# Optimization experiments

Measured on AMD Instinct MI355X. Metric: run time of the kernel, lower is better.

## Reference

```python
import jax, jax.numpy as jnp
import numpy as np

B, L, C = 2, 8192, 1536
P, W, H, F = 512, 16, 32, 128
POS = 32  # pos_channels (even, half=16 <= P-1)
EPS = 1e-5


def central_mask_features(seq_len, feat):
    # static numpy construction (matches torch central_mask_features)
    half = feat // 2
    rel = np.arange(2 * seq_len - 1, dtype=np.float64) - (seq_len - 1)
    widths = np.arange(half, dtype=np.float64) + np.geomspace(1, seq_len - half + 1, half, endpoint=False)
    onehot = (widths[None, :] > np.abs(rel)[:, None]).astype(np.float32)
    sign = np.sign(rel)[:, None].astype(np.float32)
    return jnp.asarray(np.concatenate([onehot, onehot * sign], axis=-1))  # [2P-1, POS]


def relative_shift(x):
    # x: [B, H, S, 2S-1] -> [B, H, S, S]
    b, h, s, d = x.shape
    x = jnp.pad(x, ((0, 0), (0, 0), (0, 0), (1, 0)))
    x = x.reshape(b, h, d + 1, s)[:, :, 1:, :].reshape(b, h, s, d)
    return x[..., :s]


def setup_inputs() -> dict:
    key = jax.random.key(0)
    ks = jax.random.split(key, 12)
    s = 0.02
    return {
        "x": jax.random.normal(ks[0], (B, L, C), jnp.float32),
        "norm_scale": jnp.ones((C,), jnp.float32),
        "norm_ms": jnp.ones((C,), jnp.float32),
        "Wq": jax.random.normal(ks[1], (C, H * F), jnp.float32) * s,
        "Wk": jax.random.normal(ks[2], (C, H * F), jnp.float32) * s,
        "Wp": jax.random.normal(ks[3], (POS, H * F), jnp.float32) * s,
        "bp": jax.random.normal(ks[4], (H * F,), jnp.float32) * s,
        "q_r_bias": jnp.zeros((1, 1, H, F), jnp.float32),
        "k_r_bias": jnp.zeros((1, 1, H, F), jnp.float32),
        "Wyq": jax.random.normal(ks[5], (C, F), jnp.float32) * s,
        "Wyk": jax.random.normal(ks[6], (C, F), jnp.float32) * s,
        "Wout": jax.random.normal(ks[7], (H, F), jnp.float32) * s,
        "bout": jax.random.normal(ks[8], (F,), jnp.float32) * s,
    }


def reference(x, norm_scale, norm_ms, Wq, Wk, Wp, bp, q_r_bias, k_r_bias, Wyq, Wyk, Wout, bout):
    b = x.shape[0]
    # AvgPool1d(kernel=stride=W) along sequence: [B,L,C] -> [B,P,C]
    xp = x.reshape(b, P, W, C).mean(axis=2)
    # EMA RMS batch norm (inference): per-channel rsqrt of running mean-square, learned scale
    xn = xp * (norm_scale * jax.lax.rsqrt(norm_ms + EPS))
    q = (xn @ Wq).reshape(b, P, H, F)
    k = (xn @ Wk).reshape(b, P, H, F)
    pos_feat = central_mask_features(P, POS)                     # [2P-1, POS]
    pos_enc = (pos_feat @ Wp + bp).reshape(2 * P - 1, H, F)      # [2P-1, H, F]
    rel_q = jnp.einsum('bqhc,phc->bhqp', q + q_r_bias, pos_enc) / 2
    rel_q = relative_shift(rel_q).transpose(0, 2, 3, 1)          # [B,Q,K,H]
    rel_k = jnp.einsum('bkhc,phc->bhkp', k + k_r_bias, pos_enc) / 2
    rel_k = relative_shift(rel_k).transpose(0, 2, 3, 1)          # [B,K,Q,H]
    a = jnp.einsum('bqhc,bkhc->bqkh', q, k) + 0.5 * (rel_q + rel_k.transpose(0, 2, 1, 3))
    xa = jax.nn.gelu(xn, approximate=False)
    y_q = xa @ Wyq                                               # [B,P,F]
    y_k = xa @ Wyk
    pair = jnp.einsum('bqkh,hf->bqkf', a, Wout) + bout + y_q[:, :, None, :] + y_k[:, None, :, :]
    return pair  # dropout p=0 / eval -> identity
```

## Files before the change

### kernel.cpp

```cpp
#include <hip/hip_runtime.h>
#include <math.h>

typedef unsigned short u16;
typedef unsigned int u32;
typedef __attribute__((ext_vector_type(8))) short short8;
typedef __attribute__((ext_vector_type(4))) float f32x4;
typedef __attribute__((ext_vector_type(4))) unsigned short us4;

#define BB 2
#define LL 8192
#define CC 1536
#define PP 512
#define WW 16
#define HH 32
#define FF 128
#define HF 4096
#define NBANDS 33

__device__ __forceinline__ float bf2f(u16 u){
  union { unsigned int i; float f; } v; v.i = ((unsigned int)u) << 16; return v.f;
}
__device__ __forceinline__ u16 f2bf(float f){
  union { float f; unsigned int i; } v; v.f = f;
  unsigned int x = v.i;
  return (u16)((x + 0x7fffu + ((x >> 16) & 1u)) >> 16);
}
__device__ __forceinline__ float ld_in(const void* p, size_t i, int is32){
  return is32 ? ((const float*)p)[i] : bf2f(((const u16*)p)[i]);
}
__device__ __forceinline__ int probe32(const void* ms){
  return ((const unsigned int*)ms)[0] == 0x3F800000u ? 1 : 0;
}

__global__ void k_bands(int* jt){
  int a = threadIdx.x;
  if (a < 512){
    double lw = log(497.0) / 16.0;
    int j = 0;
    for (int i = 0; i < 16; ++i){
      double w = (double)i + exp(lw * (double)i);
      if (w <= (double)a) j++;
    }
    jt[a] = j;
  }
}

__global__ void k_pool(const void* __restrict__ x, const void* __restrict__ ns,
                       const void* __restrict__ ms, u16* __restrict__ xn,
                       u16* __restrict__ xa){
  const int is32 = probe32(ms);
  int row = blockIdx.x;
  int b = row >> 9, p = row & 511;
  size_t base = ((size_t)(b*LL + p*WW)) * CC;
  for (int c4 = threadIdx.x; c4 < CC/4; c4 += 256){
    int c = c4 * 4;
    f32x4 s = (f32x4){0.f,0.f,0.f,0.f};
    if (is32){
      const float* xp = (const float*)x + base + c;
      for (int w = 0; w < WW; ++w)
        s += *(const f32x4*)(xp + (size_t)w*CC);
    } else {
      const u16* xp = (const u16*)x + base + c;
      for (int w = 0; w < WW; ++w){
        us4 v = *(const us4*)(xp + (size_t)w*CC);
        for (int u = 0; u < 4; ++u) s[u] += bf2f(v[u]);
      }
    }
    us4 on, oa;
    for (int u = 0; u < 4; ++u){
      float xp4 = s[u] * (1.f/16.f);
      float sc = ld_in(ns, c+u, is32) * rsqrtf(ld_in(ms, c+u, is32) + 1e-5f);
      float v = xp4 * sc;
      on[u] = f2bf(v);
      float g = 0.5f * v * (1.f + erff(v * 0.70710678118654752f));
      oa[u] = f2bf(g);
    }
    *(us4*)&xn[(size_t)row*CC + c] = on;
    *(us4*)&xa[(size_t)row*CC + c] = oa;
  }
}

__global__ void k_transpose(const void* __restrict__ in, u16* __restrict__ out,
                            int R, int Ccols, const void* __restrict__ msp){
  const int is32 = probe32(msp);
  __shared__ u16 tbuf[32][33];
  int c0 = blockIdx.x * 32, r0 = blockIdx.y * 32;
  int tx = threadIdx.x & 31, ty = threadIdx.x >> 5;
  for (int p = 0; p < 4; ++p)
    tbuf[ty + p*8][tx] = f2bf(ld_in(in, (size_t)(r0 + ty + p*8)*Ccols + c0 + tx, is32));
  __syncthreads();
  for (int p = 0; p < 4; ++p)
    out[(size_t)(c0 + ty + p*8)*R + r0 + tx] = tbuf[tx][ty + p*8];
}

__launch_bounds__(256)
__global__ void k_gemm(const u16* __restrict__ A, const u16* __restrict__ BT0,
                       const u16* __restrict__ BT1, u16* __restrict__ C0,
                       u16* __restrict__ C1){
  const u16* BT = blockIdx.z ? BT1 : BT0;
  u16* Cc = blockIdx.z ? C1 : C0;
  __shared__ u16 As[128*40];
  __shared__ u16 Bs[128*40];
  const int n0 = blockIdx.x * 128, m0 = blockIdx.y * 128;
  const int t = threadIdx.x, lane = t & 63, wave = t >> 6;
  const int lm = lane & 15, lq = lane >> 4;
  const int srow = t >> 1, scol = (t & 1) << 4;
  f32x4 acc[2][8];
  for (int a = 0; a < 2; ++a)
    for (int b = 0; b < 8; ++b) acc[a][b] = (f32x4){0.f,0.f,0.f,0.f};
  for (int k0 = 0; k0 < CC; k0 += 32){
    short8 va0 = *(const short8*)&A [(size_t)(m0+srow)*CC + k0 + scol];
    short8 va1 = *(const short8*)&A [(size_t)(m0+srow)*CC + k0 + scol + 8];
    short8 vb0 = *(const short8*)&BT[(size_t)(n0+srow)*CC + k0 + scol];
    short8 vb1 = *(const short8*)&BT[(size_t)(n0+srow)*CC + k0 + scol + 8];
    *(short8*)&As[srow*40 + scol]     = va0;
    *(short8*)&As[srow*40 + scol + 8] = va1;
    *(short8*)&Bs[srow*40 + scol]     = vb0;
    *(short8*)&Bs[srow*40 + scol + 8] = vb1;
    __syncthreads();
    short8 af[2], bfr[8];
    af[0] = *(const short8*)&As[(wave*32 + lm)*40 + lq*8];
    af[1] = *(const short8*)&As[(wave*32 + 16 + lm)*40 + lq*8];
    for (int nt = 0; nt < 8; ++nt)
      bfr[nt] = *(const short8*)&Bs[(nt*16 + lm)*40 + lq*8];
    for (int mt = 0; mt < 2; ++mt)
      for (int nt = 0; nt < 8; ++nt)
        acc[mt][nt] = __builtin_amdgcn_mfma_f32_16x16x32_bf16(af[mt], bfr[nt], acc[mt][nt], 0, 0, 0);
    __syncthreads();
  }
  for (int mt = 0; mt < 2; ++mt)
    for (int nt = 0; nt < 8; ++nt)
      for (int r = 0; r < 4; ++r){
        int gr = m0 + wave*32 + mt*16 + lq*4 + r;
        int gc = n0 + nt*16 + lm;
        Cc[(size_t)gr*HF + gc] = f2bf(acc[mt][nt][r]);
      }
}

__launch_bounds__(256)
__global__ void k_ygemm(const u16* __restrict__ A, const u16* __restrict__ BT,
                        float* __restrict__ yq, float* __restrict__ yk){
  __shared__ u16 As[128*40];
  __shared__ u16 Bs[128*40];
  const int n0 = blockIdx.x * 128, m0 = blockIdx.y * 128;
  const int t = threadIdx.x, lane = t & 63, wave = t >> 6;
  const int lm = lane & 15, lq = lane >> 4;
  const int srow = t >> 1, scol = (t & 1) << 4;
  f32x4 acc[2][8];
  for (int a = 0; a < 2; ++a)
    for (int b = 0; b < 8; ++b) acc[a][b] = (f32x4){0.f,0.f,0.f,0.f};
  for (int k0 = 0; k0 < CC; k0 += 32){
    short8 va0 = *(const short8*)&A [(size_t)(m0+srow)*CC + k0 + scol];
    short8 va1 = *(const short8*)&A [(size_t)(m0+srow)*CC + k0 + scol + 8];
    short8 vb0 = *(const short8*)&BT[(size_t)(n0+srow)*CC + k0 + scol];
    short8 vb1 = *(const short8*)&BT[(size_t)(n0+srow)*CC + k0 + scol + 8];
    *(short8*)&As[srow*40 + scol]     = va0;
    *(short8*)&As[srow*40 + scol + 8] = va1;
    *(short8*)&Bs[srow*40 + scol]     = vb0;
    *(short8*)&Bs[srow*40 + scol + 8] = vb1;
    __syncthreads();
    short8 af[2], bfr[8];
    af[0] = *(const short8*)&As[(wave*32 + lm)*40 + lq*8];
    af[1] = *(const short8*)&As[(wave*32 + 16 + lm)*40 + lq*8];
    for (int nt = 0; nt < 8; ++nt)
      bfr[nt] = *(const short8*)&Bs[(nt*16 + lm)*40 + lq*8];
    for (int mt = 0; mt < 2; ++mt)
      for (int nt = 0; nt < 8; ++nt)
        acc[mt][nt] = __builtin_amdgcn_mfma_f32_16x16x32_bf16(af[mt], bfr[nt], acc[mt][nt], 0, 0, 0);
    __syncthreads();
  }
  for (int mt = 0; mt < 2; ++mt)
    for (int nt = 0; nt < 8; ++nt)
      for (int r = 0; r < 4; ++r){
        int gr = m0 + wave*32 + mt*16 + lq*4 + r;
        int gc = n0 + nt*16 + lm;
        if (gc < FF) yq[(size_t)gr*FF + gc] = acc[mt][nt][r];
        else         yk[(size_t)gr*FF + gc - FF] = acc[mt][nt][r];
      }
}

__launch_bounds__(256)
__global__ void k_rel(const u16* __restrict__ qk, const void* __restrict__ rbias,
                      const void* __restrict__ Wp, const void* __restrict__ bp,
                      float* __restrict__ Dg, const void* __restrict__ msp){
  const int is32 = probe32(msp);
  __shared__ u16 As[128*136];
  __shared__ u16 Bs[48*136];
  const int r0 = blockIdx.x * 128;
  const int h  = blockIdx.y;
  const int t = threadIdx.x, lane = t & 63, wave = t >> 6;
  const int lm = lane & 15, lq = lane >> 4;

  for (int v = 0; v < 8; ++v){
    int idx = (t + v*256) * 8;
    int r = idx >> 7, c = idx & 127;
    short8 s8 = *(const short8*)&qk[(size_t)(r0 + r)*HF + h*FF + c];
    short8 o;
    for (int j = 0; j < 8; ++j)
      o[j] = (short)f2bf(bf2f((u16)s8[j]) + ld_in(rbias, (size_t)h*FF + c + j, is32));
    *(short8*)&As[r*136 + c] = o;
  }
  for (int idx = t; idx < 48*128; idx += 256){
    int i = idx >> 7, c = idx & 127;
    float v;
    if (i < 32)       v = ld_in(Wp, (size_t)i*HF + h*FF + c, is32);
    else if (i == 32) v = ld_in(bp, (size_t)h*FF + c, is32);
    else              v = 0.f;
    Bs[i*136 + c] = f2bf(v);
  }
  __syncthreads();

  f32x4 acc[2][3];
  for (int mt = 0; mt < 2; ++mt)
    for (int nt = 0; nt < 3; ++nt) acc[mt][nt] = (f32x4){0.f,0.f,0.f,0.f};
  for (int ks = 0; ks < 4; ++ks){
    short8 af[2], bfr[3];
    for (int mt = 0; mt < 2; ++mt)
      af[mt] = *(const short8*)&As[(wave*32 + mt*16 + lm)*136 + ks*32 + lq*8];
    for (int nt = 0; nt < 3; ++nt)
      bfr[nt] = *(const short8*)&Bs[(nt*16 + lm)*136 + ks*32 + lq*8];
    for (int mt = 0; mt < 2; ++mt)
      for (int nt = 0; nt < 3; ++nt)
        acc[mt][nt] = __builtin_amdgcn_mfma_f32_16x16x32_bf16(af[mt], bfr[nt], acc[mt][nt], 0, 0, 0);
  }
  for (int mt = 0; mt < 2; ++mt)
    for (int nt = 0; nt < 3; ++nt)
      for (int rr = 0; rr < 4; ++rr){
        int row = r0 + wave*32 + mt*16 + lq*4 + rr;
        int i = nt*16 + lm;
        if (i < 33)
          Dg[((size_t)row*32 + h)*33 + i] = acc[mt][nt][rr];
      }
}

__launch_bounds__(256)
__global__ void k_coef(const float* __restrict__ Dg, const float* __restrict__ yrow,
                       const void* __restrict__ Wo, const void* __restrict__ bout,
                       u16* __restrict__ Cout, const void* __restrict__ msp){
  const int is32 = probe32(msp);
  __shared__ float A1[4*32*17];
  __shared__ float A2[4*32*17];
  __shared__ float A0[4*32];
  __shared__ u16 coef[144*40];
  const int row0 = blockIdx.x * 4;
  const int t = threadIdx.x;

  {
    int r = t >> 6, h = (t >> 1) & 31, sel = t & 1;
    size_t dbase = ((size_t)(row0 + r)*32 + h)*33 + sel*16;
    float d[16];
    for (int j = 0; j < 16; ++j) d[j] = Dg[dbase + j];
    float* Aout = sel ? A2 : A1;
    int base = (r*32 + h)*17;
    float run = 0.f;
    for (int j = 16; j >= 0; --j){
      Aout[base + j] = run;
      if (j > 0) run += d[j-1];
    }
    if (!sel) A0[r*32 + h] = Dg[dbase + 32];
  }
  __syncthreads();
  for (int m = t; m < 144*32; m += 256){
    int h = m & 31; int row = m >> 5;
    if (row >= 132){ coef[row*40 + h] = 0; continue; }
    int r = row / 33; int band = row - r*33;
    float a0 = A0[r*32 + h];
    int base = (r*32 + h)*17;
    float val;
    if (band == 0)       val = A1[base] + a0;
    else if (band <= 16) val = A1[base + band] + A2[base + band] + a0;
    else                 val = A1[base + band - 16] - A2[base + band - 16] + a0;
    coef[row*40 + h] = f2bf(0.25f * val);
  }
  __syncthreads();
  const int lane = t & 63, wave = t >> 6, lm = lane & 15, lq = lane >> 4;
  short8 wf[8];
  float bo[8];
  for (int ft = 0; ft < 8; ++ft){
    short8 v;
    for (int j = 0; j < 8; ++j)
      v[j] = (short)f2bf(ld_in(Wo, (size_t)(lq*8 + j)*FF + ft*16 + lm, is32));
    wf[ft] = v;
    bo[ft] = 0.5f * ld_in(bout, ft*16 + lm, is32);
  }
  for (int mt = wave; mt < 9; mt += 4){
    short8 af = *(const short8*)&coef[(mt*16 + lm)*40 + lq*8];
    f32x4 d[8];
    for (int ft = 0; ft < 8; ++ft)
      d[ft] = __builtin_amdgcn_mfma_f32_16x16x32_bf16(af, wf[ft], (f32x4){0.f,0.f,0.f,0.f}, 0, 0, 0);
    for (int rr = 0; rr < 4; ++rr){
      int row = mt*16 + lq*4 + rr;
      if (row < 132){
        int r = row / 33; int band = row - r*33;
        const float* yr = yrow + (size_t)(row0 + r)*FF;
        u16* co = Cout + ((size_t)(row0 + r)*NBANDS + band)*FF;
        for (int ft = 0; ft < 8; ++ft){
          int f = ft*16 + lm;
          co[f] = f2bf(d[ft][rr] + yr[f] + bo[ft]);
        }
      }
    }
  }
}

__launch_bounds__(512, 4)
__global__ void k_pair(const u16* __restrict__ qb, const u16* __restrict__ kbm,
                       const u16* __restrict__ Cq, const u16* __restrict__ Ck,
                       const void* __restrict__ Wo, const int* __restrict__ jt,
                       float* __restrict__ out, const void* __restrict__ msp){
  const int is32 = probe32(msp);
  __shared__ u16 atile[1024*32];
  __shared__ int jt_lds[512];
  const int bz = blockIdx.z;
  const int flat = blockIdx.y * 16 + blockIdx.x;
  const int swz = (flat & 7) * 32 + (flat >> 3);
  const int q0 = (swz >> 4) * 32, k0 = (swz & 15) * 32;
  const int t = threadIdx.x, lane = t & 63, wave = t >> 6;
  const int lm = lane & 15, lq = lane >> 4;
  const u16* qbase = qb  + (size_t)(bz*PP + q0)*HF;
  const u16* kbase = kbm + (size_t)(bz*PP + k0)*HF;
  u32* atile32 = (u32*)atile;
  jt_lds[t] = jt[t];
  for (int hp = 0; hp < 2; ++hp){
    f32x4 acc2[2][2][2];
    for (int e = 0; e < 2; ++e){
      int h = wave*4 + hp*2 + e;
      short8 af[2][4], bfr[2][4];
      for (int qm = 0; qm < 2; ++qm)
        for (int ks = 0; ks < 4; ++ks)
          af[qm][ks] = *(const short8*)&qbase[(size_t)(qm*16 + lm)*HF + h*FF + ks*32 + lq*8];
      for (int kn = 0; kn < 2; ++kn)
        for (int ks = 0; ks < 4; ++ks)
          bfr[kn][ks] = *(const short8*)&kbase[(size_t)(kn*16 + lm)*HF + h*FF + ks*32 + lq*8];
      for (int qm = 0; qm < 2; ++qm)
        for (int kn = 0; kn < 2; ++kn){
          f32x4 acc = (f32x4){0.f,0.f,0.f,0.f};
          for (int ks = 0; ks < 4; ++ks)
            acc = __builtin_amdgcn_mfma_f32_16x16x32_bf16(af[qm][ks], bfr[kn][ks], acc, 0, 0, 0);
          acc2[e][qm][kn] = acc;
        }
    }
    int h0 = wave*4 + hp*2;
    int hg = h0 >> 3, hl0 = h0 & 7;
    for (int qm = 0; qm < 2; ++qm)
      for (int kn = 0; kn < 2; ++kn)
        for (int r = 0; r < 4; ++r){
          int pair = (qm*16 + lq*4 + r)*32 + kn*16 + lm;
          int key = (pair & 3) ^ ((pair >> 7) & 3);
          u32 pk = (u32)f2bf(acc2[0][qm][kn][r]) | ((u32)f2bf(acc2[1][qm][kn][r]) << 16);
          atile32[pair*16 + ((hg ^ key) << 2) + (hl0 >> 1)] = pk;
        }
  }
  short8 wf[8];
  for (int ft = 0; ft < 8; ++ft){
    short8 v;
    for (int j = 0; j < 8; ++j)
      v[j] = (short)f2bf(ld_in(Wo, (size_t)(lq*8 + j)*FF + ft*16 + lm, is32));
    wf[ft] = v;
  }
  __syncthreads();
  const int dQK = k0 - q0;
  auto mkaddr = [&](int rr, const u16*& cqr, const u16*& ckr, float*& orw){
    int pr = (wave*8 + rr)*16 + lm;
    int qi = pr >> 5, ki = pr & 31;
    int dd = dQK + ki - qi;
    int ad = dd < 0 ? -dd : dd;
    int j = jt_lds[ad];
    int cqb, ckb;
    if (dd == 0){ cqb = 0; ckb = 0; }
    else if (dd > 0){ cqb = j; ckb = 16 + j; }
    else { cqb = 16 + j; ckb = j; }
    int Q = q0 + qi, Kg = k0 + ki;
    cqr = Cq + ((size_t)((bz*PP + Q)*NBANDS + cqb))*FF + lq*4;
    ckr = Ck + ((size_t)((bz*PP + Kg)*NBANDS + ckb))*FF + lq*4;
    orw = out + ((size_t)(bz*PP + Q)*PP + Kg)*FF + lq*4;
  };
  us4 cqA[4], ckA[4], cqB[4], ckB[4];
  const u16 *cq_cur, *ck_cur; float *o_cur;
  mkaddr(0, cq_cur, ck_cur, o_cur);
#pragma unroll
  for (int f4 = 0; f4 < 4; ++f4){
    cqA[f4] = *(const us4*)&cq_cur[f4*16];
    ckA[f4] = *(const us4*)&ck_cur[f4*16];
  }
#pragma unroll
  for (int rr = 0; rr < 8; ++rr){
    int pr = (wave*8 + rr)*16 + lm;
    int key = (pr & 3) ^ ((pr >> 7) & 3);
    short8 afr = *(const short8*)&atile[pr*32 + ((lq ^ key) << 3)];
#pragma unroll
    for (int f4 = 0; f4 < 4; ++f4){
      cqB[f4] = *(const us4*)&cq_cur[(4 + f4)*16];
      ckB[f4] = *(const us4*)&ck_cur[(4 + f4)*16];
    }
#pragma unroll
    for (int f4 = 0; f4 < 4; ++f4){
      f32x4 d = __builtin_amdgcn_mfma_f32_16x16x32_bf16(wf[f4], afr, (f32x4){0.f,0.f,0.f,0.f}, 0, 0, 0);
      f32x4 o;
      for (int u = 0; u < 4; ++u)
        o[u] = d[u] + bf2f(cqA[f4][u]) + bf2f(ckA[f4][u]);
      *(f32x4*)&o_cur[f4*16] = o;
    }
    const u16 *cq_nxt = cq_cur, *ck_nxt = ck_cur; float *o_nxt = o_cur;
    if (rr < 7){
      mkaddr(rr + 1, cq_nxt, ck_nxt, o_nxt);
#pragma unroll
      for (int f4 = 0; f4 < 4; ++f4){
        cqA[f4] = *(const us4*)&cq_nxt[f4*16];
        ckA[f4] = *(const us4*)&ck_nxt[f4*16];
      }
    }
#pragma unroll
    for (int f4 = 0; f4 < 4; ++f4){
      f32x4 d = __builtin_amdgcn_mfma_f32_16x16x32_bf16(wf[4 + f4], afr, (f32x4){0.f,0.f,0.f,0.f}, 0, 0, 0);
      f32x4 o;
      for (int u = 0; u < 4; ++u)
        o[u] = d[u] + bf2f(cqB[f4][u]) + bf2f(ckB[f4][u]);
      *(f32x4*)&o_cur[(4 + f4)*16] = o;
    }
    cq_cur = cq_nxt; ck_cur = ck_nxt; o_cur = o_nxt;
  }
}

extern "C" void kernel_launch(void* const* d_in, const int* in_sizes, int n_in,
                              void* d_out, int out_size, void* d_ws, size_t ws_size,
                              hipStream_t stream){
  const void* x   = d_in[0];
  const void* ns  = d_in[1];
  const void* ms  = d_in[2];
  const void* Wq  = d_in[3];
  const void* Wk  = d_in[4];
  const void* Wp  = d_in[5];
  const void* bp  = d_in[6];
  const void* qrb = d_in[7];
  const void* krb = d_in[8];
  const void* Wyq = d_in[9];
  const void* Wyk = d_in[10];
  const void* Wo  = d_in[11];
  const void* bo  = d_in[12];
  float* out = (float*)d_out;

  char* ws = (char*)d_ws;
  size_t off = 0;
  auto take = [&](size_t bytes) -> char* {
    char* p = ws + off;
    off += (bytes + 255) & ~(size_t)255;
    return p;
  };
  u16*  xn   = (u16*)take((size_t)1024*CC*2);
  u16*  xa   = (u16*)take((size_t)1024*CC*2);
  u16*  qbuf = (u16*)take((size_t)1024*HF*2);
  u16*  kbuf = (u16*)take((size_t)1024*HF*2);
  u16*  WqT  = (u16*)take((size_t)HF*CC*2);
  u16*  WkT  = (u16*)take((size_t)HF*CC*2);
  u16*  WyT  = (u16*)take((size_t)2*FF*CC*2);
  float* yq  = (float*)take((size_t)1024*FF*4);
  float* yk  = (float*)take((size_t)1024*FF*4);
  u16*  Cqb  = (u16*)take((size_t)1024*NBANDS*FF*2);
  u16*  Ckb  = (u16*)take((size_t)1024*NBANDS*FF*2);
  int*  jt   = (int*)take((size_t)512*4);
  float* Dq = (float*)WqT;
  float* Dk = (float*)WkT;

  hipLaunchKernelGGL(k_bands, dim3(1), dim3(512), 0, stream, jt);
  hipLaunchKernelGGL(k_pool, dim3(1024), dim3(256), 0, stream, x, ns, ms, xn, xa);
  hipLaunchKernelGGL(k_transpose, dim3(128, 48), dim3(256), 0, stream, Wq, WqT, CC, HF, ms);
  hipLaunchKernelGGL(k_transpose, dim3(128, 48), dim3(256), 0, stream, Wk, WkT, CC, HF, ms);
  hipLaunchKernelGGL(k_transpose, dim3(4, 48), dim3(256), 0, stream, Wyq, WyT, CC, FF, ms);
  hipLaunchKernelGGL(k_transpose, dim3(4, 48), dim3(256), 0, stream, Wyk, WyT + (size_t)FF*CC, CC, FF, ms);
  hipLaunchKernelGGL(k_gemm, dim3(32, 8, 2), dim3(256), 0, stream, xn, WqT, WkT, qbuf, kbuf);
  hipLaunchKernelGGL(k_ygemm, dim3(2, 8), dim3(256), 0, stream, xa, WyT, yq, yk);
  hipLaunchKernelGGL(k_rel, dim3(8, 32), dim3(256), 0, stream, qbuf, qrb, Wp, bp, Dq, ms);
  hipLaunchKernelGGL(k_rel, dim3(8, 32), dim3(256), 0, stream, kbuf, krb, Wp, bp, Dk, ms);
  hipLaunchKernelGGL(k_coef, dim3(256), dim3(256), 0, stream, Dq, yq, Wo, bo, Cqb, ms);
  hipLaunchKernelGGL(k_coef, dim3(256), dim3(256), 0, stream, Dk, yk, Wo, bo, Ckb, ms);
  hipLaunchKernelGGL(k_pair, dim3(16, 16, 2), dim3(512), 0, stream, qbuf, kbuf, Cqb, Ckb, Wo, jt, out, ms);
}
```

Baseline: 702.0 us.

## Use direct global-to-LDS loads with XOR swizzle in GEMMs, vectorize coef epilogue

The two projection GEMMs now stage A/B tiles with global_load_lds 16-byte transfers into an unpadded, XOR-swizzled LDS layout. This bypasses the VGPR round-trip and removes the padding, while the swizzle is meant to avoid bank conflicts. The rel kernel hoists the bias loads out of its loop. The coef kernel swaps the MFMA operands so each lane owns 4 consecutive output features, which allows vectorized y loads and 8-byte bf16 stores. The risks are correctness of the swizzle and LDS-DMA addressing, and the remaining full-barrier, single-buffer structure.

```diff
diff --git a/kernel.cpp b/kernel.cpp
--- a/kernel.cpp
+++ b/kernel.cpp
@@ -16,6 +16,10 @@
 #define FF 128
 #define HF 4096
 #define NBANDS 33
+
+#define GLD16(g, l) __builtin_amdgcn_global_load_lds( \
+    (const __attribute__((address_space(1))) void*)(g), \
+    (__attribute__((address_space(3))) void*)(l), 16, 0, 0)
 
 __device__ __forceinline__ float bf2f(u16 u){
   union { unsigned int i; float f; } v; v.i = ((unsigned int)u) << 16; return v.f;
@@ -99,30 +103,36 @@
                        u16* __restrict__ C1){
   const u16* BT = blockIdx.z ? BT1 : BT0;
   u16* Cc = blockIdx.z ? C1 : C0;
-  __shared__ u16 As[128*40];
-  __shared__ u16 Bs[128*40];
+  __shared__ u16 As[128*32];
+  __shared__ u16 Bs[128*32];
   const int n0 = blockIdx.x * 128, m0 = blockIdx.y * 128;
   const int t = threadIdx.x, lane = t & 63, wave = t >> 6;
   const int lm = lane & 15, lq = lane >> 4;
-  const int srow = t >> 1, scol = (t & 1) << 4;
+  const int sub = lane >> 2;
+  const int chs = lane & 3;
   f32x4 acc[2][8];
   for (int a = 0; a < 2; ++a)
     for (int b = 0; b < 8; ++b) acc[a][b] = (f32x4){0.f,0.f,0.f,0.f};
   for (int k0 = 0; k0 < CC; k0 += 32){
-    short8 va0 = *(const short8*)&A [(size_t)(m0+srow)*CC + k0 + scol];
-    short8 va1 = *(const short8*)&A [(size_t)(m0+srow)*CC + k0 + scol + 8];
-    short8 vb0 = *(const short8*)&BT[(size_t)(n0+srow)*CC + k0 + scol];
-    short8 vb1 = *(const short8*)&BT[(size_t)(n0+srow)*CC + k0 + scol + 8];
-    *(short8*)&As[srow*40 + scol]     = va0;
-    *(short8*)&As[srow*40 + scol + 8] = va1;
-    *(short8*)&Bs[srow*40 + scol]     = vb0;
-    *(short8*)&Bs[srow*40 + scol + 8] = vb1;
+    for (int c = 0; c < 2; ++c){
+      int chunk = wave*2 + c;
+      int row = chunk*16 + sub;
+      int gch = chs ^ ((row >> 1) & 3);
+      GLD16(&A [(size_t)(m0+row)*CC + k0 + gch*8], &As[chunk*512]);
+      GLD16(&BT[(size_t)(n0+row)*CC + k0 + gch*8], &Bs[chunk*512]);
+    }
     __syncthreads();
     short8 af[2], bfr[8];
-    af[0] = *(const short8*)&As[(wave*32 + lm)*40 + lq*8];
-    af[1] = *(const short8*)&As[(wave*32 + 16 + lm)*40 + lq*8];
-    for (int nt = 0; nt < 8; ++nt)
-      bfr[nt] = *(const short8*)&Bs[(nt*16 + lm)*40 + lq*8];
+    {
+      int r0r = wave*32 + lm;
+      af[0] = *(const short8*)&As[r0r*32 + ((lq ^ ((r0r>>1)&3)) << 3)];
+      int r1r = wave*32 + 16 + lm;
+      af[1] = *(const short8*)&As[r1r*32 + ((lq ^ ((r1r>>1)&3)) << 3)];
+    }
+    for (int nt = 0; nt < 8; ++nt){
+      int br = nt*16 + lm;
+      bfr[nt] = *(const short8*)&Bs[br*32 + ((lq ^ ((br>>1)&3)) << 3)];
+    }
     for (int mt = 0; mt < 2; ++mt)
       for (int nt = 0; nt < 8; ++nt)
         acc[mt][nt] = __builtin_amdgcn_mfma_f32_16x16x32_bf16(af[mt], bfr[nt], acc[mt][nt], 0, 0, 0);
@@ -140,30 +150,36 @@
 __launch_bounds__(256)
 __global__ void k_ygemm(const u16* __restrict__ A, const u16* __restrict__ BT,
                         float* __restrict__ yq, float* __restrict__ yk){
-  __shared__ u16 As[128*40];
-  __shared__ u16 Bs[128*40];
+  __shared__ u16 As[128*32];
+  __shared__ u16 Bs[128*32];
   const int n0 = blockIdx.x * 128, m0 = blockIdx.y * 128;
   const int t = threadIdx.x, lane = t & 63, wave = t >> 6;
   const int lm = lane & 15, lq = lane >> 4;
-  const int srow = t >> 1, scol = (t & 1) << 4;
+  const int sub = lane >> 2;
+  const int chs = lane & 3;
   f32x4 acc[2][8];
   for (int a = 0; a < 2; ++a)
     for (int b = 0; b < 8; ++b) acc[a][b] = (f32x4){0.f,0.f,0.f,0.f};
   for (int k0 = 0; k0 < CC; k0 += 32){
-    short8 va0 = *(const short8*)&A [(size_t)(m0+srow)*CC + k0 + scol];
-    short8 va1 = *(const short8*)&A [(size_t)(m0+srow)*CC + k0 + scol + 8];
-    short8 vb0 = *(const short8*)&BT[(size_t)(n0+srow)*CC + k0 + scol];
-    short8 vb1 = *(const short8*)&BT[(size_t)(n0+srow)*CC + k0 + scol + 8];
-    *(short8*)&As[srow*40 + scol]     = va0;
-    *(short8*)&As[srow*40 + scol + 8] = va1;
-    *(short8*)&Bs[srow*40 + scol]     = vb0;
-    *(short8*)&Bs[srow*40 + scol + 8] = vb1;
+    for (int c = 0; c < 2; ++c){
+      int chunk = wave*2 + c;
+      int row = chunk*16 + sub;
+      int gch = chs ^ ((row >> 1) & 3);
+      GLD16(&A [(size_t)(m0+row)*CC + k0 + gch*8], &As[chunk*512]);
+      GLD16(&BT[(size_t)(n0+row)*CC + k0 + gch*8], &Bs[chunk*512]);
+    }
     __syncthreads();
     short8 af[2], bfr[8];
-    af[0] = *(const short8*)&As[(wave*32 + lm)*40 + lq*8];
-    af[1] = *(const short8*)&As[(wave*32 + 16 + lm)*40 + lq*8];
-    for (int nt = 0; nt < 8; ++nt)
-      bfr[nt] = *(const short8*)&Bs[(nt*16 + lm)*40 + lq*8];
+    {
+      int r0r = wave*32 + lm;
+      af[0] = *(const short8*)&As[r0r*32 + ((lq ^ ((r0r>>1)&3)) << 3)];
+      int r1r = wave*32 + 16 + lm;
+      af[1] = *(const short8*)&As[r1r*32 + ((lq ^ ((r1r>>1)&3)) << 3)];
+    }
+    for (int nt = 0; nt < 8; ++nt){
+      int br = nt*16 + lm;
+      bfr[nt] = *(const short8*)&Bs[br*32 + ((lq ^ ((br>>1)&3)) << 3)];
+    }
     for (int mt = 0; mt < 2; ++mt)
       for (int nt = 0; nt < 8; ++nt)
         acc[mt][nt] = __builtin_amdgcn_mfma_f32_16x16x32_bf16(af[mt], bfr[nt], acc[mt][nt], 0, 0, 0);
@@ -191,14 +207,19 @@
   const int t = threadIdx.x, lane = t & 63, wave = t >> 6;
   const int lm = lane & 15, lq = lane >> 4;
 
-  for (int v = 0; v < 8; ++v){
-    int idx = (t + v*256) * 8;
-    int r = idx >> 7, c = idx & 127;
-    short8 s8 = *(const short8*)&qk[(size_t)(r0 + r)*HF + h*FF + c];
-    short8 o;
+  {
+    const int cA = (t*8) & 127;
+    float rb[8];
     for (int j = 0; j < 8; ++j)
-      o[j] = (short)f2bf(bf2f((u16)s8[j]) + ld_in(rbias, (size_t)h*FF + c + j, is32));
-    *(short8*)&As[r*136 + c] = o;
+      rb[j] = ld_in(rbias, (size_t)h*FF + cA + j, is32);
+    for (int v = 0; v < 8; ++v){
+      int r = ((t + v*256) * 8) >> 7;
+      short8 s8 = *(const short8*)&qk[(size_t)(r0 + r)*HF + h*FF + cA];
+      short8 o;
+      for (int j = 0; j < 8; ++j)
+        o[j] = (short)f2bf(bf2f((u16)s8[j]) + rb[j]);
+      *(short8*)&As[r*136 + cA] = o;
+    }
   }
   for (int idx = t; idx < 48*128; idx += 256){
     int i = idx >> 7, c = idx & 127;
@@ -275,29 +296,33 @@
   __syncthreads();
   const int lane = t & 63, wave = t >> 6, lm = lane & 15, lq = lane >> 4;
   short8 wf[8];
-  float bo[8];
+  f32x4 bo4[8];
   for (int ft = 0; ft < 8; ++ft){
     short8 v;
     for (int j = 0; j < 8; ++j)
       v[j] = (short)f2bf(ld_in(Wo, (size_t)(lq*8 + j)*FF + ft*16 + lm, is32));
     wf[ft] = v;
-    bo[ft] = 0.5f * ld_in(bout, ft*16 + lm, is32);
+    int f0v = ft*16 + lq*4;
+    for (int u = 0; u < 4; ++u)
+      bo4[ft][u] = 0.5f * ld_in(bout, f0v + u, is32);
   }
   for (int mt = wave; mt < 9; mt += 4){
-    short8 af = *(const short8*)&coef[(mt*16 + lm)*40 + lq*8];
+    int row = mt*16 + lm;
+    short8 af = *(const short8*)&coef[row*40 + lq*8];
     f32x4 d[8];
     for (int ft = 0; ft < 8; ++ft)
-      d[ft] = __builtin_amdgcn_mfma_f32_16x16x32_bf16(af, wf[ft], (f32x4){0.f,0.f,0.f,0.f}, 0, 0, 0);
-    for (int rr = 0; rr < 4; ++rr){
-      int row = mt*16 + lq*4 + rr;
-      if (row < 132){
-        int r = row / 33; int band = row - r*33;
-        const float* yr = yrow + (size_t)(row0 + r)*FF;
-        u16* co = Cout + ((size_t)(row0 + r)*NBANDS + band)*FF;
-        for (int ft = 0; ft < 8; ++ft){
-          int f = ft*16 + lm;
-          co[f] = f2bf(d[ft][rr] + yr[f] + bo[ft]);
-        }
+      d[ft] = __builtin_amdgcn_mfma_f32_16x16x32_bf16(wf[ft], af, (f32x4){0.f,0.f,0.f,0.f}, 0, 0, 0);
+    if (row < 132){
+      int r = row / 33; int band = row - r*33;
+      const float* yr = yrow + (size_t)(row0 + r)*FF;
+      u16* co = Cout + ((size_t)(row0 + r)*NBANDS + band)*FF;
+      for (int ft = 0; ft < 8; ++ft){
+        int f0v = ft*16 + lq*4;
+        f32x4 yv = *(const f32x4*)&yr[f0v];
+        us4 ov;
+        for (int u = 0; u < 4; ++u)
+          ov[u] = f2bf(d[ft][u] + yv[u] + bo4[ft][u]);
+        *(us4*)&co[f0v] = ov;
       }
     }
   }
```

Result: faster. 658.2 us (-6.2%).
